# Optimization experiments

Hardware: AMD Instinct MI355X
Metric: run time of the kernel (lower is better)

## Reference

```python
import jax, jax.numpy as jnp
import numpy as np

K = 3  # kernel_size per dim
DIM = 3
NUM_K = K ** DIM  # 27
# the 2^3 corner offsets of the linear B-spline support
OFFS = np.array([[(s >> d) & 1 for d in range(DIM)] for s in range(2 ** DIM)], dtype=np.int32)  # [8,3]
STRIDES = np.array([K ** d for d in range(DIM)], dtype=np.int32)  # [1,3,9]


def bspline_basis(pseudo):
    """Open B-spline basis, degree 1. pseudo: [E,3] in [0,1]. Returns basis [E,8], kidx [E,8]."""
    v = pseudo * (K - 1)
    i0 = jnp.clip(jnp.floor(v), 0, K - 2)
    f = v - i0  # fractional part in [0,1]
    i0 = i0.astype(jnp.int32)
    offs = jnp.asarray(OFFS)  # [8,3]
    w = jnp.where(offs[None].astype(bool), f[:, None, :], 1.0 - f[:, None, :])  # [E,8,3]
    basis = jnp.prod(w, axis=-1)  # [E,8]
    kidx = jnp.sum((i0[:, None, :] + offs[None]) * jnp.asarray(STRIDES)[None, None, :], axis=-1)  # [E,8]
    return basis, kidx


def spline_conv(x, src, dst, pseudo, W, Wroot, b, num_nodes):
    """SplineConv (degree 1, mean aggregation, root weight + bias)."""
    cout = W.shape[-1]
    xW = jnp.einsum('nc,kco->nko', x, W)  # [N,27,Cout]
    basis, kidx = bspline_basis(pseudo)
    flat = src[:, None] * NUM_K + kidx  # [E,8]
    g = xW.reshape(-1, cout)[flat]  # [E,8,Cout] -- dominant gather
    msg = jnp.einsum('es,eso->eo', basis, g)  # [E,Cout]
    agg = jax.ops.segment_sum(msg, dst, num_segments=num_nodes)
    cnt = jax.ops.segment_sum(jnp.ones((src.shape[0],), x.dtype), dst, num_segments=num_nodes)
    return agg / jnp.maximum(cnt, 1.0)[:, None] + x @ Wroot + b


def seg_max(x, seg, num_segments):
    m = jax.ops.segment_max(x, seg, num_segments=num_segments)
    return jnp.where(jnp.isfinite(m), m, 0.0)  # empty clusters -> 0


def setup_inputs() -> dict:
    key = jax.random.key(0)
    ks = jax.random.split(key, 16)
    N, E, B = 80000, 1280000, 16
    N1, N2 = N // 2, N1 if False else (N // 2) // 2  # N1=40000, N2=20000
    N1 = N // 2
    N2 = N1 // 2
    x = jax.random.normal(ks[0], (N, 2), dtype=jnp.float32)
    edge_index = jax.random.randint(ks[1], (2, E), 0, N, dtype=jnp.int32)
    edge_attr = jax.random.uniform(ks[2], (E, 3), dtype=jnp.float32)
    batch = jnp.sort(jax.random.randint(ks[3], (N,), 0, B, dtype=jnp.int32))
    cluster1 = jax.random.randint(ks[4], (N,), 0, N1, dtype=jnp.int32)
    cluster2 = jax.random.randint(ks[5], (N1,), 0, N2, dtype=jnp.int32)
    W1 = jax.random.normal(ks[6], (NUM_K, 2, 8), dtype=jnp.float32) * 0.3
    root1 = jax.random.normal(ks[7], (2, 8), dtype=jnp.float32) * 0.3
    b1 = jnp.zeros((8,), jnp.float32)
    W2 = jax.random.normal(ks[8], (NUM_K, 8, 16), dtype=jnp.float32) * 0.2
    root2 = jax.random.normal(ks[9], (8, 16), dtype=jnp.float32) * 0.2
    b2 = jnp.zeros((16,), jnp.float32)
    fc1_w = jax.random.normal(ks[10], (16, 64), dtype=jnp.float32) * 0.2
    fc1_b = jnp.zeros((64,), jnp.float32)
    fc2_w = jax.random.normal(ks[11], (64, 1), dtype=jnp.float32) * 0.2
    fc2_b = jnp.zeros((1,), jnp.float32)
    return dict(x=x, edge_index=edge_index, edge_attr=edge_attr, batch=batch,
                cluster1=cluster1, cluster2=cluster2,
                W1=W1, root1=root1, b1=b1, W2=W2, root2=root2, b2=b2,
                fc1_w=fc1_w, fc1_b=fc1_b, fc2_w=fc2_w, fc2_b=fc2_b)


def reference(x, edge_index, edge_attr, batch, cluster1, cluster2,
              W1, root1, b1, W2, root2, b2, fc1_w, fc1_b, fc2_w, fc2_b):
    N = x.shape[0]
    N1 = cluster1.max() * 0 + cluster2.shape[0]  # static: 40000
    N1 = cluster2.shape[0]
    N2 = N1 // 2
    B = 16
    src, dst = edge_index[0], edge_index[1]
    # level 1: SplineConv + ELU
    h = jax.nn.elu(spline_conv(x, src, dst, edge_attr, W1, root1, b1, N))
    # max_pool with precomputed cluster assignment (replaces graclus)
    x1 = seg_max(h, cluster1, N1)
    batch1 = jnp.maximum(jax.ops.segment_max(batch, cluster1, num_segments=N1), 0)
    src2 = cluster1[src]
    dst2 = cluster1[dst]
    # level 2: SplineConv + ELU on coarsened graph
    h2 = jax.nn.elu(spline_conv(x1, src2, dst2, edge_attr, W2, root2, b2, N1))
    x2 = seg_max(h2, cluster2, N2)
    batch2 = jnp.maximum(jax.ops.segment_max(batch1, cluster2, num_segments=N2), 0)
    # scatter_mean over graphs
    s = jax.ops.segment_sum(x2, batch2, num_segments=B)
    c = jax.ops.segment_sum(jnp.ones((N2,), x.dtype), batch2, num_segments=B)
    g = s / jnp.maximum(c, 1.0)[:, None]  # [B,16]
    g = jax.nn.elu(g @ fc1_w + fc1_b)  # dropout is identity in eval mode
    return jax.nn.elu(g @ fc2_w + fc2_b)  # [B,1]
```

## Files before the change

kernel.cpp:

```cpp
#include <hip/hip_runtime.h>
#include <hip/hip_fp16.h>
#include <math.h>


__device__ __forceinline__ float eluf(float x) {
    return x > 0.f ? x : (expf(x) - 1.f);
}

__device__ __forceinline__ float hlo(int v) {
    __half2 h; *(int*)&h = v; return __low2float(h);
}
__device__ __forceinline__ float hhi(int v) {
    __half2 h; *(int*)&h = v; return __high2float(h);
}

typedef _Float16 half2v __attribute__((ext_vector_type(2)));

__device__ __forceinline__ half2v uash2(unsigned u) {
    half2v h; *(unsigned*)&h = u; return h;
}

__device__ __forceinline__ float dot2f(half2v a, half2v b, float c) {
#if __has_builtin(__builtin_amdgcn_fdot2)
    return __builtin_amdgcn_fdot2(a, b, c, false);
#else
    return c + (float)a[0] * (float)b[0] + (float)a[1] * (float)b[1];
#endif
}

#define W1_STRIDE 20
#define W2H_STRIDE 68


__global__ __launch_bounds__(256) void hist_kernel(
    const int* __restrict__ ei, const int* __restrict__ cluster1,
    const int* __restrict__ cluster2,
    int* __restrict__ deg, int* __restrict__ rank,
    int* __restrict__ cdeg, int* __restrict__ rankC,
    int* __restrict__ c2deg, int* __restrict__ rank2,
    int E, int N, int N1)
{
    int i = blockIdx.x * 256 + threadIdx.x;
    if (i < E)  rank[i]  = atomicAdd(&deg[ei[E + i]], 1);
    if (i < N)  rankC[i] = atomicAdd(&cdeg[cluster1[i]], 1);
    if (i < N1) rank2[i] = atomicAdd(&c2deg[cluster2[i]], 1);
}

#define SCAN_CHUNK 4096

__global__ __launch_bounds__(256) void scan_a(
    const int* __restrict__ in0, int* __restrict__ out0, int* __restrict__ aux0, int L0, int nb0,
    const int* __restrict__ in1, int* __restrict__ out1, int* __restrict__ aux1, int L1, int nb1,
    const int* __restrict__ in2, int* __restrict__ out2, int* __restrict__ aux2, int L2)
{
    int b = blockIdx.x;
    const int* in; int* out; int* aux; int L;
    if (b < nb0)            { in = in0; out = out0; aux = aux0; L = L0; }
    else if (b < nb0 + nb1) { b -= nb0; in = in1; out = out1; aux = aux1; L = L1; }
    else                    { b -= nb0 + nb1; in = in2; out = out2; aux = aux2; L = L2; }

    __shared__ int ls[256];
    int t = threadIdx.x;
    int base = b * SCAN_CHUNK + t * 16;
    int v[16];
    int s = 0;
#pragma unroll
    for (int j = 0; j < 16; ++j) {
        int val = (base + j < L) ? in[base + j] : 0;
        v[j] = s;
        s += val;
    }
    ls[t] = s;
    __syncthreads();
    for (int off = 1; off < 256; off <<= 1) {
        int tv = (t >= off) ? ls[t - off] : 0;
        __syncthreads();
        ls[t] += tv;
        __syncthreads();
    }
    int excl = ls[t] - s;
#pragma unroll
    for (int j = 0; j < 16; ++j)
        if (base + j < L) out[base + j] = excl + v[j];
    if (t == 255) aux[b] = ls[255];
}

__global__ __launch_bounds__(64) void scan_b(
    int* __restrict__ aux0, int nb0, int* __restrict__ off0, int L0,
    int* __restrict__ aux1, int nb1, int* __restrict__ off1, int L1,
    int* __restrict__ aux2, int nb2, int* __restrict__ off2, int L2)
{
    if (threadIdx.x != 0) return;
    int* aux; int nb; int* off; int L;
    if (blockIdx.x == 0)      { aux = aux0; nb = nb0; off = off0; L = L0; }
    else if (blockIdx.x == 1) { aux = aux1; nb = nb1; off = off1; L = L1; }
    else                      { aux = aux2; nb = nb2; off = off2; L = L2; }
    int run = 0;
    for (int j = 0; j < nb; ++j) { int tv = aux[j]; aux[j] = run; run += tv; }
    off[L] = run;
}

__global__ __launch_bounds__(256) void scan_c(
    int* __restrict__ out0, const int* __restrict__ aux0, int L0, int nb0,
    int* __restrict__ out1, const int* __restrict__ aux1, int L1, int nb1,
    int* __restrict__ out2, const int* __restrict__ aux2, int L2)
{
    int b = blockIdx.x;
    int* out; const int* aux; int L;
    if (b < nb0)            { out = out0; aux = aux0; L = L0; }
    else if (b < nb0 + nb1) { b -= nb0; out = out1; aux = aux1; L = L1; }
    else                    { b -= nb0 + nb1; out = out2; aux = aux2; L = L2; }
    int add = aux[b];
    int base = b * SCAN_CHUNK + threadIdx.x * 16;
#pragma unroll
    for (int j = 0; j < 16; ++j)
        if (base + j < L) out[base + j] += add;
}

__global__ __launch_bounds__(256) void scatA_kernel(
    const int* __restrict__ ei, const float* __restrict__ attr,
    const int* __restrict__ cluster1, const int* __restrict__ cluster2,
    const int* __restrict__ doffs, const int* __restrict__ rank,
    const int* __restrict__ coff, const int* __restrict__ rankC,
    const int* __restrict__ c2off, const int* __restrict__ rank2,
    int* __restrict__ nidx, int* __restrict__ n1idx,
    int4* __restrict__ meta, int E, int N, int N1)
{
    int i = blockIdx.x * 256 + threadIdx.x;
    if (i < E) {
        int s = ei[i], d = ei[E + i];
        int p = doffs[d] + rank[i];

        float vx = attr[3 * i] * 2.f, vy = attr[3 * i + 1] * 2.f, vz = attr[3 * i + 2] * 2.f;
        float ix = fmaxf(fminf(floorf(vx), 1.f), 0.f);
        float iy = fmaxf(fminf(floorf(vy), 1.f), 0.f);
        float iz = fmaxf(fminf(floorf(vz), 1.f), 0.f);
        float fx = vx - ix, fy = vy - iy, fz = vz - iz;
        int ixi = (int)ix, iyi = (int)iy, izi = (int)iz;
        int ibase = ixi + 3 * iyi + 9 * izi;
        int slot  = ixi + 2 * iyi + 4 * izi;

        unsigned hfx = __half_as_ushort(__float2half_rn(fx));
        unsigned hfy = __half_as_ushort(__float2half_rn(fy));
        unsigned hfz = __half_as_ushort(__float2half_rn(fz));
        int s2 = cluster1[s];
        meta[p] = make_int4(s2 | (slot << 16), s | (ibase << 17),
                            (int)(hfx | (hfy << 16)), (int)hfz);
    }
    if (i < N)  nidx[coff[cluster1[i]] + rankC[i]] = i;
    if (i < N1) n1idx[c2off[cluster2[i]] + rank2[i]] = i;
}

__global__ __launch_bounds__(256) void edge1m_kernel(
    const int4* __restrict__ meta, const float2* __restrict__ x,
    const float* __restrict__ W1, float* __restrict__ msg1, int E)
{
    __shared__ float lw[27 * W1_STRIDE];
    for (int i = threadIdx.x; i < 27 * 16; i += 256)
        lw[(i >> 4) * W1_STRIDE + (i & 15)] = W1[i];
    __syncthreads();

    int t = blockIdx.x * 256 + threadIdx.x;
    if (t >= E * 8) return;
    int p = t >> 3, ch = t & 7;
    int4 m = meta[p];
    int src = m.y & 0x1FFFF, ibase = m.y >> 17;
    float fx = hlo(m.z), fy = hhi(m.z), fz = hlo(m.w);
    float2 xv = x[src];
    float wx0 = 1.f - fx, wy0 = 1.f - fy, wz0 = 1.f - fz;
    float ca = 0.f, cb = 0.f;
#pragma unroll
    for (int j = 0; j < 8; ++j) {
        int cx = j & 1, cy = (j >> 1) & 1, cz = j >> 2;
        float w = (cx ? fx : wx0) * (cy ? fy : wy0) * (cz ? fz : wz0);
        int k = ibase + cx + 3 * cy + 9 * cz;
        ca += w * lw[k * W1_STRIDE + ch];
        cb += w * lw[k * W1_STRIDE + 8 + ch];
    }
    msg1[t] = ca * xv.x + cb * xv.y;
}

__global__ __launch_bounds__(256) void reduce1_kernel(
    const int* __restrict__ doffs, const float* __restrict__ msg1,
    float* __restrict__ M1, int N)
{
    int t = blockIdx.x * 256 + threadIdx.x;
    if (t >= N * 8) return;
    int d = t >> 3, ch = t & 7;
    int beg = doffs[d], end = doffs[d + 1];
    float acc = 0.f;
    for (int p = beg; p < end; ++p)
        acc += msg1[p * 8 + ch];
    M1[t] = acc / fmaxf((float)(end - beg), 1.f);
}

__global__ __launch_bounds__(256) void node1_kernel(
    const int* __restrict__ coff, const int* __restrict__ nidx,
    const float* __restrict__ M1, const float2* __restrict__ x,
    const float* __restrict__ root1, const float* __restrict__ b1,
    const int* __restrict__ batch,
    float* __restrict__ x1c, int* __restrict__ batch1, int N1)
{
    int t = blockIdx.x * 256 + threadIdx.x;
    if (t >= N1 * 8) return;
    int c = t >> 3, ch = t & 7;
    int cb = coff[c], ce = coff[c + 1];
    float r0 = root1[ch], r1 = root1[8 + ch], bo = b1[ch];
    float hm = -INFINITY;
    int bm = 0;
    for (int idx = cb; idx < ce; ++idx) {
        int d = nidx[idx];
        float2 xv = x[d];
        float h = eluf(M1[d * 8 + ch] + xv.x * r0 + xv.y * r1 + bo);
        hm = fmaxf(hm, h);
        bm = max(bm, batch[d]);
    }
    if (ce == cb) hm = 0.f;
    x1c[t] = hm;
    if (ch == 0) batch1[c] = bm;
}

__global__ __launch_bounds__(256) void edge2m_kernel(
    const int4* __restrict__ meta, const float* __restrict__ x1c,
    const float* __restrict__ W2, unsigned short* __restrict__ msg2h, int E)
{
    __shared__ unsigned lwh[27 * W2H_STRIDE];
    for (int i = threadIdx.x; i < 27 * 64; i += 256) {
        int k = i >> 6, r = i & 63;
        int o = r >> 2, c2 = r & 3;
        float a = W2[(k * 8 + 2 * c2) * 16 + o];
        float b = W2[(k * 8 + 2 * c2 + 1) * 16 + o];
        __half2 h = __floats2half2_rn(a, b);
        lwh[k * W2H_STRIDE + r] = *(unsigned*)&h;
    }
    __syncthreads();

    int t = blockIdx.x * 256 + threadIdx.x;
    if (t >= E * 4) return;
    int p = t >> 2, oq = t & 3;
    int4 m = meta[p];
    int s2 = m.x & 0xFFFF;
    int ibase = m.y >> 17;
    float fx = hlo(m.z), fy = hhi(m.z), fz = hlo(m.w);

    const float4* xr4 = (const float4*)&x1c[s2 * 8];
    float4 xa = xr4[0], xb = xr4[1];
    half2v xh0, xh1, xh2, xh3;
    xh0[0] = (_Float16)xa.x; xh0[1] = (_Float16)xa.y;
    xh1[0] = (_Float16)xa.z; xh1[1] = (_Float16)xa.w;
    xh2[0] = (_Float16)xb.x; xh2[1] = (_Float16)xb.y;
    xh3[0] = (_Float16)xb.z; xh3[1] = (_Float16)xb.w;

    float wx0 = 1.f - fx, wy0 = 1.f - fy, wz0 = 1.f - fz;
    float acc0 = 0.f, acc1 = 0.f, acc2 = 0.f, acc3 = 0.f;
#pragma unroll
    for (int j = 0; j < 8; ++j) {
        int cx = j & 1, cy = (j >> 1) & 1, cz = j >> 2;
        float w = (cx ? fx : wx0) * (cy ? fy : wy0) * (cz ? fz : wz0);
        int k = ibase + cx + 3 * cy + 9 * cz;
        const unsigned* base = &lwh[k * W2H_STRIDE + oq * 16];
        uint4 v0 = *(const uint4*)(base);
        uint4 v1 = *(const uint4*)(base + 4);
        uint4 v2 = *(const uint4*)(base + 8);
        uint4 v3 = *(const uint4*)(base + 12);
        float s0 = dot2f(xh0, uash2(v0.x), dot2f(xh1, uash2(v0.y),
                   dot2f(xh2, uash2(v0.z), dot2f(xh3, uash2(v0.w), 0.f))));
        float s1 = dot2f(xh0, uash2(v1.x), dot2f(xh1, uash2(v1.y),
                   dot2f(xh2, uash2(v1.z), dot2f(xh3, uash2(v1.w), 0.f))));
        float s2v = dot2f(xh0, uash2(v2.x), dot2f(xh1, uash2(v2.y),
                    dot2f(xh2, uash2(v2.z), dot2f(xh3, uash2(v2.w), 0.f))));
        float s3 = dot2f(xh0, uash2(v3.x), dot2f(xh1, uash2(v3.y),
                   dot2f(xh2, uash2(v3.z), dot2f(xh3, uash2(v3.w), 0.f))));
        acc0 = fmaf(w, s0, acc0);
        acc1 = fmaf(w, s1, acc1);
        acc2 = fmaf(w, s2v, acc2);
        acc3 = fmaf(w, s3, acc3);
    }
    __half2 lo = __floats2half2_rn(acc0, acc1);
    __half2 hi = __floats2half2_rn(acc2, acc3);
    uint2 outv = make_uint2(*(unsigned*)&lo, *(unsigned*)&hi);
    *(uint2*)&msg2h[p * 16 + oq * 4] = outv;
}

__global__ __launch_bounds__(256) void reduce2_kernel(
    const int* __restrict__ coff, const int* __restrict__ nidx,
    const int* __restrict__ doffs, const unsigned short* __restrict__ msg2h,
    float* __restrict__ M2, int N1)
{
    int t = blockIdx.x * 256 + threadIdx.x;
    if (t >= N1 * 16) return;
    int c = t >> 4, o = t & 15;
    float acc = 0.f;
    int cnt = 0;
    int cb = coff[c], ce = coff[c + 1];
    for (int idx = cb; idx < ce; ++idx) {
        int d = nidx[idx];
        int beg = doffs[d], end = doffs[d + 1];
        cnt += end - beg;
        for (int p = beg; p < end; ++p)
            acc += __half2float(__ushort_as_half(msg2h[p * 16 + o]));
    }
    M2[t] = acc / fmaxf((float)cnt, 1.f);
}

__global__ __launch_bounds__(256) void node2_kernel(
    const int* __restrict__ c2off, const int* __restrict__ n1idx,
    const float* __restrict__ M2, const float* __restrict__ x1c,
    const float* __restrict__ root2, const float* __restrict__ b2,
    const int* __restrict__ batch1,
    float* __restrict__ gsum, float* __restrict__ gcnt, int N2)
{
    __shared__ float ls[16 * 16];
    __shared__ float lc[16];
    for (int i = threadIdx.x; i < 256; i += 256) ls[i] = 0.f;
    if (threadIdx.x < 16) lc[threadIdx.x] = 0.f;
    __syncthreads();

    int c2 = blockIdx.x * 256 + threadIdx.x;
    if (c2 < N2) {
        int cb = c2off[c2], ce = c2off[c2 + 1];
        float hm[16];
#pragma unroll
        for (int o = 0; o < 16; ++o) hm[o] = -INFINITY;
        int bm = 0;
        for (int idx = cb; idx < ce; ++idx) {
            int n1 = n1idx[idx];
            const float4* xr4 = (const float4*)&x1c[n1 * 8];
            float4 xa = xr4[0], xb = xr4[1];
            float xr[8] = {xa.x, xa.y, xa.z, xa.w, xb.x, xb.y, xb.z, xb.w};
#pragma unroll
            for (int o = 0; o < 16; ++o) {
                float v = M2[n1 * 16 + o] + b2[o];
#pragma unroll
                for (int c8 = 0; c8 < 8; ++c8) v += xr[c8] * root2[c8 * 16 + o];
                hm[o] = fmaxf(hm[o], eluf(v));
            }
            bm = max(bm, batch1[n1]);
        }
        if (ce == cb) {
#pragma unroll
            for (int o = 0; o < 16; ++o) hm[o] = 0.f;
        }
#pragma unroll
        for (int o = 0; o < 16; ++o) atomicAdd(&ls[bm * 16 + o], hm[o]);
        atomicAdd(&lc[bm], 1.f);
    }
    __syncthreads();
    for (int i = threadIdx.x; i < 256; i += 256) unsafeAtomicAdd(&gsum[i], ls[i]);
    if (threadIdx.x < 16) unsafeAtomicAdd(&gcnt[threadIdx.x], lc[threadIdx.x]);
}

__global__ __launch_bounds__(256) void head_kernel(
    const float* __restrict__ gsum, const float* __restrict__ gcnt,
    const float* __restrict__ fc1_w, const float* __restrict__ fc1_b,
    const float* __restrict__ fc2_w, const float* __restrict__ fc2_b,
    float* __restrict__ out, int B)
{
    __shared__ float g[16 * 16];
    __shared__ float h1[16 * 64];
    int t = threadIdx.x;
    if (t < B * 16) {
        int b = t >> 4;
        g[t] = gsum[t] / fmaxf(gcnt[b], 1.f);
    }
    __syncthreads();
    for (int j = t; j < B * 64; j += 256) {
        int b = j >> 6, jj = j & 63;
        float s = fc1_b[jj];
#pragma unroll
        for (int c = 0; c < 16; ++c) s += g[b * 16 + c] * fc1_w[c * 64 + jj];
        h1[j] = eluf(s);
    }
    __syncthreads();
    if (t < B) {
        float s = fc2_b[0];
#pragma unroll
        for (int j = 0; j < 64; ++j) s += h1[t * 64 + j] * fc2_w[j];
        out[t] = eluf(s);
    }
}

extern "C" void kernel_launch(void* const* d_in, const int* in_sizes, int n_in,
                              void* d_out, int out_size, void* d_ws, size_t ws_size,
                              hipStream_t stream)
{
    const float* x        = (const float*)d_in[0];
    const int*   ei       = (const int*)  d_in[1];
    const float* attr     = (const float*)d_in[2];
    const int*   batch    = (const int*)  d_in[3];
    const int*   cluster1 = (const int*)  d_in[4];
    const int*   cluster2 = (const int*)  d_in[5];
    const float* W1       = (const float*)d_in[6];
    const float* root1    = (const float*)d_in[7];
    const float* b1       = (const float*)d_in[8];
    const float* W2       = (const float*)d_in[9];
    const float* root2    = (const float*)d_in[10];
    const float* b2       = (const float*)d_in[11];
    const float* fc1_w    = (const float*)d_in[12];
    const float* fc1_b    = (const float*)d_in[13];
    const float* fc2_w    = (const float*)d_in[14];
    const float* fc2_b    = (const float*)d_in[15];

    const int N  = in_sizes[0] / 2;
    const int E  = in_sizes[1] / 2;
    const int N1 = in_sizes[5];
    const int N2 = N1 / 2;
    const int B  = out_size;

    const int nb0 = (N  + SCAN_CHUNK - 1) / SCAN_CHUNK;
    const int nb1 = (N1 + SCAN_CHUNK - 1) / SCAN_CHUNK;
    const int nb2 = (N2 + SCAN_CHUNK - 1) / SCAN_CHUNK;

    int* wi = (int*)d_ws;
    size_t off = 0;
    auto alloc = [&](size_t n, size_t align = 1) {
        off = (off + align - 1) & ~(align - 1);
        size_t r = off; off += n; return r;
    };
    int*   deg    = wi + alloc(N);
    int*   cdeg   = wi + alloc(N1);
    int*   c2deg  = wi + alloc(N2);
    float* gsum   = (float*)(wi + alloc((size_t)B * 16));
    float* gcnt   = (float*)(wi + alloc(B));
    const size_t zcount = off;
    int*   doffs  = wi + alloc(N + 1);
    int*   coff   = wi + alloc(N1 + 1);
    int*   c2off  = wi + alloc(N2 + 1);
    int*   auxA   = wi + alloc(nb0);
    int*   auxB   = wi + alloc(nb1);
    int*   auxC   = wi + alloc(nb2);
    int*   rank   = wi + alloc(E);
    int*   rankC  = wi + alloc(N);
    int*   rank2  = wi + alloc(N1);
    int*   nidx   = wi + alloc(N);
    int*   n1idx  = wi + alloc(N1);
    int4*  meta   = (int4*)(wi + alloc((size_t)E * 4, 4));
    float* msg1   = (float*)(wi + alloc((size_t)E * 8, 4));
    unsigned short* msg2h = (unsigned short*)msg1;
    float* M1     = (float*)(wi + alloc((size_t)N * 8, 4));
    float* x1c    = (float*)(wi + alloc((size_t)N1 * 8, 4));
    int*   batch1 = wi + alloc(N1);
    float* M2     = (float*)(wi + alloc((size_t)N1 * 16, 4));
    (void)ws_size;

    hipMemsetAsync(d_ws, 0, zcount * sizeof(int), stream);

    const int eb = (E + 255) / 256;
    hist_kernel<<<eb, 256, 0, stream>>>(ei, cluster1, cluster2,
                                        deg, rank, cdeg, rankC, c2deg, rank2, E, N, N1);
    scan_a<<<nb0 + nb1 + nb2, 256, 0, stream>>>(deg, doffs, auxA, N, nb0,
                                                cdeg, coff, auxB, N1, nb1,
                                                c2deg, c2off, auxC, N2);
    scan_b<<<3, 64, 0, stream>>>(auxA, nb0, doffs, N,
                                 auxB, nb1, coff, N1,
                                 auxC, nb2, c2off, N2);
    scan_c<<<nb0 + nb1 + nb2, 256, 0, stream>>>(doffs, auxA, N, nb0,
                                                coff, auxB, N1, nb1,
                                                c2off, auxC, N2);
    scatA_kernel<<<eb, 256, 0, stream>>>(ei, attr, cluster1, cluster2,
                                         doffs, rank, coff, rankC, c2off, rank2,
                                         nidx, n1idx, meta, E, N, N1);
    edge1m_kernel<<<(E * 8 + 255) / 256, 256, 0, stream>>>(
        meta, (const float2*)x, W1, msg1, E);
    reduce1_kernel<<<(N * 8 + 255) / 256, 256, 0, stream>>>(doffs, msg1, M1, N);
    node1_kernel<<<(N1 * 8 + 255) / 256, 256, 0, stream>>>(
        coff, nidx, M1, (const float2*)x, root1, b1, batch, x1c, batch1, N1);
    edge2m_kernel<<<(E * 4 + 255) / 256, 256, 0, stream>>>(
        meta, x1c, W2, msg2h, E);
    reduce2_kernel<<<(N1 * 16 + 255) / 256, 256, 0, stream>>>(
        coff, nidx, doffs, msg2h, M2, N1);
    node2_kernel<<<(N2 + 255) / 256, 256, 0, stream>>>(
        c2off, n1idx, M2, x1c, root2, b2, batch1, gsum, gcnt, N2);
    head_kernel<<<1, 256, 0, stream>>>(gsum, gcnt, fc1_w, fc1_b, fc2_w, fc2_b,
                                       (float*)d_out, B);
}
```

Baseline: 386.8 us.

## Fuse level-1 edge message computation into scatter kernel with fp16 records

```diff
diff --git a/kernel.cpp b/kernel.cpp
--- a/kernel.cpp
+++ b/kernel.cpp
@@ -117,15 +117,21 @@
         if (base + j < L) out[base + j] += add;
 }
 
-__global__ __launch_bounds__(256) void scatA_kernel(
+__global__ __launch_bounds__(256) void scatB_kernel(
     const int* __restrict__ ei, const float* __restrict__ attr,
     const int* __restrict__ cluster1, const int* __restrict__ cluster2,
+    const float2* __restrict__ x, const float* __restrict__ W1,
     const int* __restrict__ doffs, const int* __restrict__ rank,
     const int* __restrict__ coff, const int* __restrict__ rankC,
     const int* __restrict__ c2off, const int* __restrict__ rank2,
     int* __restrict__ nidx, int* __restrict__ n1idx,
-    int4* __restrict__ meta, int E, int N, int N1)
-{
+    int4* __restrict__ rec4, int E, int N, int N1)
+{
+    __shared__ float lw[27 * W1_STRIDE];
+    for (int i = threadIdx.x; i < 27 * 16; i += 256)
+        lw[(i >> 4) * W1_STRIDE + (i & 15)] = W1[i];
+    __syncthreads();
+
     int i = blockIdx.x * 256 + threadIdx.x;
     if (i < E) {
         int s = ei[i], d = ei[E + i];
@@ -136,52 +142,53 @@
         float iy = fmaxf(fminf(floorf(vy), 1.f), 0.f);
         float iz = fmaxf(fminf(floorf(vz), 1.f), 0.f);
         float fx = vx - ix, fy = vy - iy, fz = vz - iz;
-        int ixi = (int)ix, iyi = (int)iy, izi = (int)iz;
-        int ibase = ixi + 3 * iyi + 9 * izi;
-        int slot  = ixi + 2 * iyi + 4 * izi;
+        int ibase = (int)ix + 3 * (int)iy + 9 * (int)iz;
+
+        float2 xv = x[s];
+        float wxv[2] = {1.f - fx, fx}, wyv[2] = {1.f - fy, fy}, wzv[2] = {1.f - fz, fz};
+        float m[8];
+#pragma unroll
+        for (int o = 0; o < 8; ++o) m[o] = 0.f;
+#pragma unroll
+        for (int j = 0; j < 8; ++j) {
+            int cx = j & 1, cy = (j >> 1) & 1, cz = j >> 2;
+            float w = wxv[cx] * wyv[cy] * wzv[cz];
+            const float* Wk = &lw[(ibase + cx + 3 * cy + 9 * cz) * W1_STRIDE];
+            float a = w * xv.x, bb = w * xv.y;
+            const float4 wa0 = *(const float4*)&Wk[0];
+            const float4 wa1 = *(const float4*)&Wk[4];
+            const float4 wb0 = *(const float4*)&Wk[8];
+            const float4 wb1 = *(const float4*)&Wk[12];
+            m[0] += a * wa0.x + bb * wb0.x;
+            m[1] += a * wa0.y + bb * wb0.y;
+            m[2] += a * wa0.z + bb * wb0.z;
+            m[3] += a * wa0.w + bb * wb0.w;
+            m[4] += a * wa1.x + bb * wb1.x;
+            m[5] += a * wa1.y + bb * wb1.y;
+            m[6] += a * wa1.z + bb * wb1.z;
+            m[7] += a * wa1.w + bb * wb1.w;
+        }
 
         unsigned hfx = __half_as_ushort(__float2half_rn(fx));
         unsigned hfy = __half_as_ushort(__float2half_rn(fy));
         unsigned hfz = __half_as_ushort(__float2half_rn(fz));
         int s2 = cluster1[s];
-        meta[p] = make_int4(s2 | (slot << 16), s | (ibase << 17),
-                            (int)(hfx | (hfy << 16)), (int)hfz);
+        int4 ra = make_int4(s2 | (ibase << 16),
+                            (int)(hfx | (hfy << 16)), (int)hfz, 0);
+        __half2 h01 = __floats2half2_rn(m[0], m[1]);
+        __half2 h23 = __floats2half2_rn(m[2], m[3]);
+        __half2 h45 = __floats2half2_rn(m[4], m[5]);
+        __half2 h67 = __floats2half2_rn(m[6], m[7]);
+        int4 rb = make_int4(*(int*)&h01, *(int*)&h23, *(int*)&h45, *(int*)&h67);
+        rec4[2 * (size_t)p]     = ra;
+        rec4[2 * (size_t)p + 1] = rb;
     }
     if (i < N)  nidx[coff[cluster1[i]] + rankC[i]] = i;
     if (i < N1) n1idx[c2off[cluster2[i]] + rank2[i]] = i;
 }
 
-__global__ __launch_bounds__(256) void edge1m_kernel(
-    const int4* __restrict__ meta, const float2* __restrict__ x,
-    const float* __restrict__ W1, float* __restrict__ msg1, int E)
-{
-    __shared__ float lw[27 * W1_STRIDE];
-    for (int i = threadIdx.x; i < 27 * 16; i += 256)
-        lw[(i >> 4) * W1_STRIDE + (i & 15)] = W1[i];
-    __syncthreads();
-
-    int t = blockIdx.x * 256 + threadIdx.x;
-    if (t >= E * 8) return;
-    int p = t >> 3, ch = t & 7;
-    int4 m = meta[p];
-    int src = m.y & 0x1FFFF, ibase = m.y >> 17;
-    float fx = hlo(m.z), fy = hhi(m.z), fz = hlo(m.w);
-    float2 xv = x[src];
-    float wx0 = 1.f - fx, wy0 = 1.f - fy, wz0 = 1.f - fz;
-    float ca = 0.f, cb = 0.f;
-#pragma unroll
-    for (int j = 0; j < 8; ++j) {
-        int cx = j & 1, cy = (j >> 1) & 1, cz = j >> 2;
-        float w = (cx ? fx : wx0) * (cy ? fy : wy0) * (cz ? fz : wz0);
-        int k = ibase + cx + 3 * cy + 9 * cz;
-        ca += w * lw[k * W1_STRIDE + ch];
-        cb += w * lw[k * W1_STRIDE + 8 + ch];
-    }
-    msg1[t] = ca * xv.x + cb * xv.y;
-}
-
 __global__ __launch_bounds__(256) void reduce1_kernel(
-    const int* __restrict__ doffs, const float* __restrict__ msg1,
+    const int* __restrict__ doffs, const unsigned short* __restrict__ recU,
     float* __restrict__ M1, int N)
 {
     int t = blockIdx.x * 256 + threadIdx.x;
@@ -190,7 +197,7 @@
     int beg = doffs[d], end = doffs[d + 1];
     float acc = 0.f;
     for (int p = beg; p < end; ++p)
-        acc += msg1[p * 8 + ch];
+        acc += __half2float(__ushort_as_half(recU[(size_t)p * 16 + 8 + ch]));
     M1[t] = acc / fmaxf((float)(end - beg), 1.f);
 }
 
@@ -199,7 +206,8 @@
     const float* __restrict__ M1, const float2* __restrict__ x,
     const float* __restrict__ root1, const float* __restrict__ b1,
     const int* __restrict__ batch,
-    float* __restrict__ x1c, int* __restrict__ batch1, int N1)
+    float* __restrict__ x1c, unsigned short* __restrict__ x1chU,
+    int* __restrict__ batch1, int N1)
 {
     int t = blockIdx.x * 256 + threadIdx.x;
     if (t >= N1 * 8) return;
@@ -217,11 +225,12 @@
     }
     if (ce == cb) hm = 0.f;
     x1c[t] = hm;
+    x1chU[t] = __half_as_ushort(__float2half_rn(hm));
     if (ch == 0) batch1[c] = bm;
 }
 
 __global__ __launch_bounds__(256) void edge2m_kernel(
-    const int4* __restrict__ meta, const float* __restrict__ x1c,
+    const int4* __restrict__ rec4, const unsigned short* __restrict__ x1chU,
     const float* __restrict__ W2, unsigned short* __restrict__ msg2h, int E)
 {
     __shared__ unsigned lwh[27 * W2H_STRIDE];
@@ -238,18 +247,14 @@
     int t = blockIdx.x * 256 + threadIdx.x;
     if (t >= E * 4) return;
     int p = t >> 2, oq = t & 3;
-    int4 m = meta[p];
+    int4 m = rec4[2 * (size_t)p];
     int s2 = m.x & 0xFFFF;
-    int ibase = m.y >> 17;
-    float fx = hlo(m.z), fy = hhi(m.z), fz = hlo(m.w);
-
-    const float4* xr4 = (const float4*)&x1c[s2 * 8];
-    float4 xa = xr4[0], xb = xr4[1];
-    half2v xh0, xh1, xh2, xh3;
-    xh0[0] = (_Float16)xa.x; xh0[1] = (_Float16)xa.y;
-    xh1[0] = (_Float16)xa.z; xh1[1] = (_Float16)xa.w;
-    xh2[0] = (_Float16)xb.x; xh2[1] = (_Float16)xb.y;
-    xh3[0] = (_Float16)xb.z; xh3[1] = (_Float16)xb.w;
+    int ibase = (m.x >> 16) & 31;
+    float fx = hlo(m.y), fy = hhi(m.y), fz = hlo(m.z);
+
+    const uint4 xv4 = *(const uint4*)&x1chU[(size_t)s2 * 8];
+    half2v xh0 = uash2(xv4.x), xh1 = uash2(xv4.y),
+           xh2 = uash2(xv4.z), xh3 = uash2(xv4.w);
 
     float wx0 = 1.f - fx, wy0 = 1.f - fy, wz0 = 1.f - fz;
     float acc0 = 0.f, acc1 = 0.f, acc2 = 0.f, acc3 = 0.f;
@@ -279,7 +284,7 @@
     __half2 lo = __floats2half2_rn(acc0, acc1);
     __half2 hi = __floats2half2_rn(acc2, acc3);
     uint2 outv = make_uint2(*(unsigned*)&lo, *(unsigned*)&hi);
-    *(uint2*)&msg2h[p * 16 + oq * 4] = outv;
+    *(uint2*)&msg2h[(size_t)p * 16 + oq * 4] = outv;
 }
 
 __global__ __launch_bounds__(256) void reduce2_kernel(
@@ -298,7 +303,7 @@
         int beg = doffs[d], end = doffs[d + 1];
         cnt += end - beg;
         for (int p = beg; p < end; ++p)
-            acc += __half2float(__ushort_as_half(msg2h[p * 16 + o]));
+            acc += __half2float(__ushort_as_half(msg2h[(size_t)p * 16 + o]));
     }
     M2[t] = acc / fmaxf((float)cnt, 1.f);
 }
@@ -325,12 +330,12 @@
         int bm = 0;
         for (int idx = cb; idx < ce; ++idx) {
             int n1 = n1idx[idx];
-            const float4* xr4 = (const float4*)&x1c[n1 * 8];
+            const float4* xr4 = (const float4*)&x1c[(size_t)n1 * 8];
             float4 xa = xr4[0], xb = xr4[1];
             float xr[8] = {xa.x, xa.y, xa.z, xa.w, xb.x, xb.y, xb.z, xb.w};
 #pragma unroll
             for (int o = 0; o < 16; ++o) {
-                float v = M2[n1 * 16 + o] + b2[o];
+                float v = M2[(size_t)n1 * 16 + o] + b2[o];
 #pragma unroll
                 for (int c8 = 0; c8 < 8; ++c8) v += xr[c8] * root2[c8 * 16 + o];
                 hm[o] = fmaxf(hm[o], eluf(v));
@@ -434,11 +439,11 @@
     int*   rank2  = wi + alloc(N1);
     int*   nidx   = wi + alloc(N);
     int*   n1idx  = wi + alloc(N1);
-    int4*  meta   = (int4*)(wi + alloc((size_t)E * 4, 4));
-    float* msg1   = (float*)(wi + alloc((size_t)E * 8, 4));
-    unsigned short* msg2h = (unsigned short*)msg1;
+    int4*  rec4   = (int4*)(wi + alloc((size_t)E * 8, 8));
+    unsigned short* msg2h = (unsigned short*)(wi + alloc((size_t)E * 8, 4));
     float* M1     = (float*)(wi + alloc((size_t)N * 8, 4));
     float* x1c    = (float*)(wi + alloc((size_t)N1 * 8, 4));
+    unsigned short* x1chU = (unsigned short*)(wi + alloc((size_t)N1 * 4, 4));
     int*   batch1 = wi + alloc(N1);
     float* M2     = (float*)(wi + alloc((size_t)N1 * 16, 4));
     (void)ws_size;
@@ -457,16 +462,17 @@
     scan_c<<<nb0 + nb1 + nb2, 256, 0, stream>>>(doffs, auxA, N, nb0,
                                                 coff, auxB, N1, nb1,
                                                 c2off, auxC, N2);
-    scatA_kernel<<<eb, 256, 0, stream>>>(ei, attr, cluster1, cluster2,
+    scatB_kernel<<<eb, 256, 0, stream>>>(ei, attr, cluster1, cluster2,
+                                         (const float2*)x, W1,
                                          doffs, rank, coff, rankC, c2off, rank2,
-                                         nidx, n1idx, meta, E, N, N1);
-    edge1m_kernel<<<(E * 8 + 255) / 256, 256, 0, stream>>>(
-        meta, (const float2*)x, W1, msg1, E);
-    reduce1_kernel<<<(N * 8 + 255) / 256, 256, 0, stream>>>(doffs, msg1, M1, N);
+                                         nidx, n1idx, rec4, E, N, N1);
+    reduce1_kernel<<<(N * 8 + 255) / 256, 256, 0, stream>>>(
+        doffs, (const unsigned short*)rec4, M1, N);
     node1_kernel<<<(N1 * 8 + 255) / 256, 256, 0, stream>>>(
-        coff, nidx, M1, (const float2*)x, root1, b1, batch, x1c, batch1, N1);
+        coff, nidx, M1, (const float2*)x, root1, b1, batch,
+        x1c, x1chU, batch1, N1);
     edge2m_kernel<<<(E * 4 + 255) / 256, 256, 0, stream>>>(
-        meta, x1c, W2, msg2h, E);
+        rec4, x1chU, W2, msg2h, E);
     reduce2_kernel<<<(N1 * 16 + 255) / 256, 256, 0, stream>>>(
         coff, nidx, doffs, msg2h, M2, N1);
     node2_kernel<<<(N2 + 255) / 256, 256, 0, stream>>>(
```

New measurement: 358.0 us (median of 2 runs). -7.4%, faster.
